# Optimization experiments

Measured on AMD Instinct MI355X. Metric: run time of the kernel, lower is better.

The kernel has to match this reference:

```python
import jax, jax.numpy as jnp
import numpy as np

B, N, M, D = 64, 197, 65, 768


def setup_inputs() -> dict:
    key = jax.random.key(0)
    k1, k2, k3 = jax.random.split(key, 3)
    image = jax.random.normal(k1, (B, N, D), dtype=jnp.float32)
    text = jax.random.normal(k2, (B, M, D), dtype=jnp.float32)
    pm = jax.random.randint(k3, (B, M), 0, 2).astype(jnp.int32)
    pm = pm.at[:, :2].set(0)  # CLS + first real token always valid
    logit_scale = jnp.ones((), dtype=jnp.float32)
    return {"image": image, "text": text, "padding_masks": pm, "logit_scale": logit_scale}


def _ce_with_diag_labels(logits):
    # F.cross_entropy(logits, arange(B)): mean of -log_softmax diag
    return -jnp.mean(jnp.diagonal(jax.nn.log_softmax(logits, axis=-1)))


def reference(image, text, padding_masks, logit_scale):
    # include_cls_token=False: original computes full [B,B,N,M] then slices
    # [:, :, 1:, 1:]; we compute the sliced tokens directly (same math).
    img = image[:, 1:, :]                   # [B, N-1, D]
    txt = text[:, 1:, :]                    # [B, M-1, D]
    pm = padding_masks[:, 1:].astype(bool)  # [B, M-1] True = padded

    # sim[i,j,n,m] = logit_scale * <img_i,n , txt_j,m>
    sim = logit_scale * jnp.einsum('ind,jmd->ijnm', img, txt)  # [B,B,N-1,M-1]

    # Original masks with NaN along mask of batch-row i (broadcast over j,n).
    # logits_per_image: nan_to_num(-inf) -> max over m -> mean over n
    sim_img = jnp.where(pm[:, None, None, :], -jnp.inf, sim)
    logits_per_image = jnp.mean(jnp.max(sim_img, axis=3), axis=2)  # [B,B]

    # logits_per_text: max over n (NaN cols stay NaN) -> nanmean over m.
    # Equivalent masked mean over valid m (mask constant along n).
    max_n = jnp.max(sim, axis=2)                         # [B,B,M-1]
    valid = ~pm                                          # [B,M-1]
    cnt = jnp.sum(valid, axis=1).astype(sim.dtype)       # [B]
    logits_per_text = jnp.sum(
        jnp.where(valid[:, None, :], max_n, 0.0), axis=2
    ) / cnt[:, None]                                     # [B,B]

    loss = 0.5 * (_ce_with_diag_labels(logits_per_image)
                  + _ce_with_diag_labels(logits_per_text))
    targets = jnp.arange(logits_per_image.shape[0], dtype=jnp.int32)
    return loss, logits_per_image, logits_per_text, targets
```

## Files before the change

### kernel.cpp

```cpp
#include <hip/hip_runtime.h>

typedef _Float16 half8 __attribute__((ext_vector_type(8)));
typedef float floatx4 __attribute__((ext_vector_type(4)));
typedef float float4v __attribute__((ext_vector_type(4)));

#define DIM   768
#define NROW  196
#define AUNITS (64 * 13 * 24 * 64)
#define TUNITS (64 * 4 * 24 * 64)
#define A_HALFS ((size_t)AUNITS * 8)
#define BJ_HALFS (24 * 4 * 64 * 8)

__device__ __forceinline__ void gl_lds16(const _Float16* g, _Float16* l) {
  __builtin_amdgcn_global_load_lds(
      (const __attribute__((address_space(1))) unsigned int*)g,
      (__attribute__((address_space(3))) unsigned int*)l, 16, 0, 0);
}

__global__ __launch_bounds__(256) void repack(const float* __restrict__ img,
                                              const float* __restrict__ txt,
                                              _Float16* __restrict__ Apk,
                                              _Float16* __restrict__ Bpk) {
  int gid = blockIdx.x * 256 + threadIdx.x;
  const float* src;
  _Float16* dst;
  if (gid < AUNITS) {
    int l = gid & 63, g = gid >> 6;
    int s = g % 24; g /= 24;
    int tau = g % 13; int i = g / 13;
    int n = tau * 16 + (l & 15); if (n > 195) n = 195;
    src = img + (size_t)i * 197 * 768 + (size_t)(n + 1) * 768 + s * 32 + (l >> 4) * 8;
    dst = Apk + (size_t)gid * 8;
  } else {
    int u = gid - AUNITS;
    int l = u & 63, g = u >> 6;
    int ct = g & 3; g >>= 2;
    int s = g % 24; int j = g / 24;
    int m = ct * 16 + (l & 15);
    src = txt + (size_t)j * 65 * 768 + (size_t)(m + 1) * 768 + s * 32 + (l >> 4) * 8;
    dst = Bpk + (size_t)u * 8;
  }
  float4v v0 = *(const float4v*)src;
  float4v v1 = *(const float4v*)(src + 4);
  half8 h;
  h[0] = (_Float16)v0[0]; h[1] = (_Float16)v0[1]; h[2] = (_Float16)v0[2]; h[3] = (_Float16)v0[3];
  h[4] = (_Float16)v1[0]; h[5] = (_Float16)v1[1]; h[6] = (_Float16)v1[2]; h[7] = (_Float16)v1[3];
  *(half8*)dst = h;
}

__global__ __launch_bounds__(256, 2) void sim_kernel(const _Float16* __restrict__ Apk,
                                                     const _Float16* __restrict__ Bpk,
                                                     const int* __restrict__ pm,
                                                     const float* __restrict__ ls,
                                                     float* __restrict__ lpi,
                                                     float* __restrict__ lpt) {
  __shared__ _Float16 Bsh[32768];

  const int jb = blockIdx.x, i = blockIdx.y;
  const int tid = threadIdx.x;
  const int wave = tid >> 6, lane = tid & 63;
  const int r16 = lane & 15;
  const int lane8 = lane * 8;

  const _Float16* Ai = Apk + (size_t)i * 13 * 24 * 512;
  const _Float16* pA[4];
  pA[0] = Ai + (size_t)(wave)     * 24 * 512 + lane8;
  pA[1] = Ai + (size_t)(wave + 4) * 24 * 512 + lane8;
  pA[2] = Ai + (size_t)(wave + 8) * 24 * 512 + lane8;
  pA[3] = Ai + (size_t)12         * 24 * 512 + lane8;
  const _Float16* Bg = Bpk + (size_t)(2 * jb) * BJ_HALFS;

#pragma unroll
  for (int r8 = 0; r8 < 8; ++r8) {
    int u = wave * 8 + r8;
    int jj = u >> 4, rr = u & 15;
    gl_lds16(Bg + (size_t)jj * BJ_HALFS + rr * 512 + lane8,
             Bsh + jj * 8192 + rr * 512);
  }

  half8 af[2][4];
#pragma unroll
  for (int d = 0; d < 2; ++d)
#pragma unroll
    for (int t = 0; t < 4; ++t)
      af[d][t] = *(const half8*)(pA[t] + d * 512);

  floatx4 acc[2][3][4];
  floatx4 acc12[2];
  acc12[0] = (floatx4){0.f, 0.f, 0.f, 0.f};
  acc12[1] = (floatx4){0.f, 0.f, 0.f, 0.f};
#pragma unroll
  for (int jj = 0; jj < 2; ++jj)
#pragma unroll
    for (int t = 0; t < 3; ++t)
#pragma unroll
      for (int cc = 0; cc < 4; ++cc)
        acc[jj][t][cc] = (floatx4){0.f, 0.f, 0.f, 0.f};

#pragma unroll
  for (int c = 0; c < 6; ++c) {
    __syncthreads();
    if (c < 5) {
#pragma unroll
      for (int r8 = 0; r8 < 8; ++r8) {
        int u = wave * 8 + r8;
        int jj = u >> 4, rr = u & 15;
        gl_lds16(Bg + (size_t)jj * BJ_HALFS + (c + 1) * 8192 + rr * 512 + lane8,
                 Bsh + ((c + 1) & 1) * 16384 + jj * 8192 + rr * 512);
      }
    }
#pragma unroll
    for (int sc = 0; sc < 4; ++sc) {
      const int s = c * 4 + sc;
      const int base = (c & 1) * 16384 + sc * 2048 + lane8;
      half8 b0[4], b1[4];
#pragma unroll
      for (int cc = 0; cc < 4; ++cc) {
        int ct = (wave + cc) & 3;
        b0[cc] = *(const half8*)(Bsh + base + ct * 512);
        b1[cc] = *(const half8*)(Bsh + base + 8192 + ct * 512);
      }
      half8 a0 = af[s & 1][0], a1 = af[s & 1][1], a2 = af[s & 1][2], a3 = af[s & 1][3];
      if (s < 22) {
#pragma unroll
        for (int t = 0; t < 4; ++t) af[s & 1][t] = *(const half8*)(pA[t] + (s + 2) * 512);
      }
#pragma unroll
      for (int cc = 0; cc < 4; ++cc) {
        acc[0][0][cc] = __builtin_amdgcn_mfma_f32_16x16x32_f16(a0, b0[cc], acc[0][0][cc], 0, 0, 0);
        acc[0][1][cc] = __builtin_amdgcn_mfma_f32_16x16x32_f16(a1, b0[cc], acc[0][1][cc], 0, 0, 0);
        acc[0][2][cc] = __builtin_amdgcn_mfma_f32_16x16x32_f16(a2, b0[cc], acc[0][2][cc], 0, 0, 0);
        acc[1][0][cc] = __builtin_amdgcn_mfma_f32_16x16x32_f16(a0, b1[cc], acc[1][0][cc], 0, 0, 0);
        acc[1][1][cc] = __builtin_amdgcn_mfma_f32_16x16x32_f16(a1, b1[cc], acc[1][1][cc], 0, 0, 0);
        acc[1][2][cc] = __builtin_amdgcn_mfma_f32_16x16x32_f16(a2, b1[cc], acc[1][2][cc], 0, 0, 0);
      }
      acc12[0] = __builtin_amdgcn_mfma_f32_16x16x32_f16(a3, b0[0], acc12[0], 0, 0, 0);
      acc12[1] = __builtin_amdgcn_mfma_f32_16x16x32_f16(a3, b1[0], acc12[1], 0, 0, 0);
    }
  }

  const float sgl = ls[0];
  bool msk[4];
  int colc[4];
#pragma unroll
  for (int cc = 0; cc < 4; ++cc) {
    colc[cc] = ((wave + cc) & 3) * 16 + r16;
    msk[cc] = pm[i * 65 + 1 + colc[cc]] != 0;
  }

  float rowsum[2] = {0.f, 0.f};
  float cmv[2][4];
#pragma unroll
  for (int jj = 0; jj < 2; ++jj) {
#pragma unroll
    for (int t = 0; t < 3; ++t) {
#pragma unroll
      for (int r = 0; r < 4; ++r) {
        float rm = -__builtin_inff();
#pragma unroll
        for (int cc = 0; cc < 4; ++cc) {
          float v = acc[jj][t][cc][r] * sgl;
          rm = fmaxf(rm, msk[cc] ? -__builtin_inff() : v);
        }
#pragma unroll
        for (int off = 1; off < 16; off <<= 1)
          rm = fmaxf(rm, __shfl_xor(rm, off, 64));
        rowsum[jj] += rm;
      }
    }
#pragma unroll
    for (int off = 1; off < 64; off <<= 1) rowsum[jj] += __shfl_xor(rowsum[jj], off, 64);

#pragma unroll
    for (int cc = 0; cc < 4; ++cc) {
      float cm = -__builtin_inff();
#pragma unroll
      for (int t = 0; t < 3; ++t)
#pragma unroll
        for (int r = 0; r < 4; ++r)
          cm = fmaxf(cm, acc[jj][t][cc][r] * sgl);
      cm = fmaxf(cm, __shfl_xor(cm, 16, 64));
      cm = fmaxf(cm, __shfl_xor(cm, 32, 64));
      cmv[jj][cc] = cm;
    }
  }

  __syncthreads();
  float* colmaxS = (float*)Bsh;
  float* t12S    = (float*)Bsh + 512;
  float* wsumS   = (float*)Bsh + 1024;

  if (lane == 0) { wsumS[wave] = rowsum[0]; wsumS[4 + wave] = rowsum[1]; }
  if (lane < 16) {
#pragma unroll
    for (int jj = 0; jj < 2; ++jj) {
#pragma unroll
      for (int cc = 0; cc < 4; ++cc) colmaxS[jj * 256 + wave * 64 + colc[cc]] = cmv[jj][cc];
#pragma unroll
      for (int r = 0; r < 4; ++r) t12S[jj * 256 + r * 64 + wave * 16 + r16] = acc12[jj][r] * sgl;
    }
  }
  __syncthreads();

  if (tid < 128) {
    const int jj = wave;
    const int col = lane;
    bool valid = pm[i * 65 + 1 + col] == 0;
    const float* cm = colmaxS + jj * 256;
    const float* t12 = t12S + jj * 256;
    float t0 = t12[col], t1 = t12[64 + col], t2 = t12[128 + col], t3 = t12[192 + col];
    float v = fmaxf(fmaxf(cm[col], cm[64 + col]), fmaxf(cm[128 + col], cm[192 + col]));
    v = fmaxf(v, fmaxf(fmaxf(t0, t1), fmaxf(t2, t3)));
    float contrib = valid ? v : 0.f;
    float cntv = valid ? 1.f : 0.f;
    float rs0 = valid ? t0 : -__builtin_inff();
    float rs1 = valid ? t1 : -__builtin_inff();
    float rs2 = valid ? t2 : -__builtin_inff();
    float rs3 = valid ? t3 : -__builtin_inff();
#pragma unroll
    for (int off = 1; off < 64; off <<= 1) {
      contrib += __shfl_xor(contrib, off, 64);
      cntv += __shfl_xor(cntv, off, 64);
      rs0 = fmaxf(rs0, __shfl_xor(rs0, off, 64));
      rs1 = fmaxf(rs1, __shfl_xor(rs1, off, 64));
      rs2 = fmaxf(rs2, __shfl_xor(rs2, off, 64));
      rs3 = fmaxf(rs3, __shfl_xor(rs3, off, 64));
    }
    if (lane == 0) {
      int jout = 2 * jb + jj;
      lpt[i * 64 + jout] = contrib / cntv;
      float wtot = wsumS[jj * 4 + 0] + wsumS[jj * 4 + 1] + wsumS[jj * 4 + 2] + wsumS[jj * 4 + 3];
      lpi[i * 64 + jout] = (wtot * 0.0625f + rs0 + rs1 + rs2 + rs3) / 196.f;
    }
  }
}

__global__ __launch_bounds__(64) void ce_kernel(float* __restrict__ out) {
  const int t = threadIdx.x;
  const float* lpi = out + 1;
  const float* lpt = out + 1 + 4096;

  float mx = -__builtin_inff();
  for (int jj = 0; jj < 64; ++jj) mx = fmaxf(mx, lpi[t * 64 + jj]);
  float se = 0.f;
  for (int jj = 0; jj < 64; ++jj) se += __expf(lpi[t * 64 + jj] - mx);
  float ci = (mx + __logf(se)) - lpi[t * 64 + t];

  float mx2 = -__builtin_inff();
  for (int jj = 0; jj < 64; ++jj) mx2 = fmaxf(mx2, lpt[t * 64 + jj]);
  float se2 = 0.f;
  for (int jj = 0; jj < 64; ++jj) se2 += __expf(lpt[t * 64 + jj] - mx2);
  float ct_ = (mx2 + __logf(se2)) - lpt[t * 64 + t];

  float v = ci + ct_;
#pragma unroll
  for (int off = 1; off < 64; off <<= 1) v += __shfl_xor(v, off, 64);
  if (t == 0) out[0] = 0.5f * v / 64.f;
  out[1 + 8192 + t] = (float)t;
}

extern "C" void kernel_launch(void* const* d_in, const int* in_sizes, int n_in,
                              void* d_out, int out_size, void* d_ws, size_t ws_size,
                              hipStream_t stream) {
  const float* image = (const float*)d_in[0];
  const float* text  = (const float*)d_in[1];
  const int*   pm    = (const int*)d_in[2];
  const float* ls    = (const float*)d_in[3];
  float* out = (float*)d_out;

  _Float16* Apk = (_Float16*)d_ws;
  _Float16* Bpk = Apk + A_HALFS;

  repack<<<(AUNITS + TUNITS) / 256, 256, 0, stream>>>(image, text, Apk, Bpk);

  dim3 grid(32, 64);
  sim_kernel<<<grid, 256, 0, stream>>>(Apk, Bpk, pm, ls, out + 1, out + 1 + 4096);
  ce_kernel<<<1, 64, 0, stream>>>(out);
}
```

Measured before the change: 185.7 us.

## Process one text batch per block to cut registers and LDS, raise occupancy

Each sim_kernel block now handles a single text item j instead of two. This halves the accumulator registers and shrinks LDS from 64KB to 16KB, with staging done in smaller double-buffered chunks over 12 stages. The grid doubles to 64x64 and launch bounds ask for 3 blocks per CU. The trade-off is that each image A tile is now reloaded from global/L2 twice as often, so every MFMA does less reuse. The ce_kernel loops are also unrolled.

Result: slower. 194.8 us (+4.9%).

```diff
diff --git a/kernel.cpp b/kernel.cpp
--- a/kernel.cpp
+++ b/kernel.cpp
@@ -48,15 +48,15 @@
   *(half8*)dst = h;
 }
 
-__global__ __launch_bounds__(256, 2) void sim_kernel(const _Float16* __restrict__ Apk,
+__global__ __launch_bounds__(256, 3) void sim_kernel(const _Float16* __restrict__ Apk,
                                                      const _Float16* __restrict__ Bpk,
                                                      const int* __restrict__ pm,
                                                      const float* __restrict__ ls,
                                                      float* __restrict__ lpi,
                                                      float* __restrict__ lpt) {
-  __shared__ _Float16 Bsh[32768];
-
-  const int jb = blockIdx.x, i = blockIdx.y;
+  __shared__ _Float16 Bsh[8192];
+
+  const int j = blockIdx.x, i = blockIdx.y;
   const int tid = threadIdx.x;
   const int wave = tid >> 6, lane = tid & 63;
   const int r16 = lane & 15;
@@ -68,14 +68,12 @@
   pA[1] = Ai + (size_t)(wave + 4) * 24 * 512 + lane8;
   pA[2] = Ai + (size_t)(wave + 8) * 24 * 512 + lane8;
   pA[3] = Ai + (size_t)12         * 24 * 512 + lane8;
-  const _Float16* Bg = Bpk + (size_t)(2 * jb) * BJ_HALFS;
-
-#pragma unroll
-  for (int r8 = 0; r8 < 8; ++r8) {
-    int u = wave * 8 + r8;
-    int jj = u >> 4, rr = u & 15;
-    gl_lds16(Bg + (size_t)jj * BJ_HALFS + rr * 512 + lane8,
-             Bsh + jj * 8192 + rr * 512);
+  const _Float16* Bg = Bpk + (size_t)j * BJ_HALFS;
+
+#pragma unroll
+  for (int r2 = 0; r2 < 2; ++r2) {
+    int rr = wave * 2 + r2;
+    gl_lds16(Bg + rr * 512 + lane8, Bsh + rr * 512);
   }
 
   half8 af[2][4];
@@ -85,40 +83,34 @@
     for (int t = 0; t < 4; ++t)
       af[d][t] = *(const half8*)(pA[t] + d * 512);
 
-  floatx4 acc[2][3][4];
-  floatx4 acc12[2];
-  acc12[0] = (floatx4){0.f, 0.f, 0.f, 0.f};
-  acc12[1] = (floatx4){0.f, 0.f, 0.f, 0.f};
-#pragma unroll
-  for (int jj = 0; jj < 2; ++jj)
-#pragma unroll
-    for (int t = 0; t < 3; ++t)
-#pragma unroll
-      for (int cc = 0; cc < 4; ++cc)
-        acc[jj][t][cc] = (floatx4){0.f, 0.f, 0.f, 0.f};
-
-#pragma unroll
-  for (int c = 0; c < 6; ++c) {
+  floatx4 acc[3][4];
+  floatx4 acc12 = (floatx4){0.f, 0.f, 0.f, 0.f};
+#pragma unroll
+  for (int t = 0; t < 3; ++t)
+#pragma unroll
+    for (int cc = 0; cc < 4; ++cc)
+      acc[t][cc] = (floatx4){0.f, 0.f, 0.f, 0.f};
+
+#pragma unroll
+  for (int c = 0; c < 12; ++c) {
     __syncthreads();
-    if (c < 5) {
-#pragma unroll
-      for (int r8 = 0; r8 < 8; ++r8) {
-        int u = wave * 8 + r8;
-        int jj = u >> 4, rr = u & 15;
-        gl_lds16(Bg + (size_t)jj * BJ_HALFS + (c + 1) * 8192 + rr * 512 + lane8,
-                 Bsh + ((c + 1) & 1) * 16384 + jj * 8192 + rr * 512);
-      }
-    }
-#pragma unroll
-    for (int sc = 0; sc < 4; ++sc) {
-      const int s = c * 4 + sc;
-      const int base = (c & 1) * 16384 + sc * 2048 + lane8;
-      half8 b0[4], b1[4];
+    if (c < 11) {
+#pragma unroll
+      for (int r2 = 0; r2 < 2; ++r2) {
+        int rr = wave * 2 + r2;
+        gl_lds16(Bg + (c + 1) * 4096 + rr * 512 + lane8,
+                 Bsh + ((c + 1) & 1) * 4096 + rr * 512);
+      }
+    }
+#pragma unroll
+    for (int sc = 0; sc < 2; ++sc) {
+      const int s = c * 2 + sc;
+      const int base = (c & 1) * 4096 + sc * 2048 + lane8;
+      half8 b0[4];
 #pragma unroll
       for (int cc = 0; cc < 4; ++cc) {
         int ct = (wave + cc) & 3;
         b0[cc] = *(const half8*)(Bsh + base + ct * 512);
-        b1[cc] = *(const half8*)(Bsh + base + 8192 + ct * 512);
       }
       half8 a0 = af[s & 1][0], a1 = af[s & 1][1], a2 = af[s & 1][2], a3 = af[s & 1][3];
       if (s < 22) {
@@ -127,15 +119,11 @@
       }
 #pragma unroll
       for (int cc = 0; cc < 4; ++cc) {
-        acc[0][0][cc] = __builtin_amdgcn_mfma_f32_16x16x32_f16(a0, b0[cc], acc[0][0][cc], 0, 0, 0);
-        acc[0][1][cc] = __builtin_amdgcn_mfma_f32_16x16x32_f16(a1, b0[cc], acc[0][1][cc], 0, 0, 0);
-        acc[0][2][cc] = __builtin_amdgcn_mfma_f32_16x16x32_f16(a2, b0[cc], acc[0][2][cc], 0, 0, 0);
-        acc[1][0][cc] = __builtin_amdgcn_mfma_f32_16x16x32_f16(a0, b1[cc], acc[1][0][cc], 0, 0, 0);
-        acc[1][1][cc] = __builtin_amdgcn_mfma_f32_16x16x32_f16(a1, b1[cc], acc[1][1][cc], 0, 0, 0);
-        acc[1][2][cc] = __builtin_amdgcn_mfma_f32_16x16x32_f16(a2, b1[cc], acc[1][2][cc], 0, 0, 0);
-      }
-      acc12[0] = __builtin_amdgcn_mfma_f32_16x16x32_f16(a3, b0[0], acc12[0], 0, 0, 0);
-      acc12[1] = __builtin_amdgcn_mfma_f32_16x16x32_f16(a3, b1[0], acc12[1], 0, 0, 0);
+        acc[0][cc] = __builtin_amdgcn_mfma_f32_16x16x32_f16(a0, b0[cc], acc[0][cc], 0, 0, 0);
+        acc[1][cc] = __builtin_amdgcn_mfma_f32_16x16x32_f16(a1, b0[cc], acc[1][cc], 0, 0, 0);
+        acc[2][cc] = __builtin_amdgcn_mfma_f32_16x16x32_f16(a2, b0[cc], acc[2][cc], 0, 0, 0);
+      }
+      acc12 = __builtin_amdgcn_mfma_f32_16x16x32_f16(a3, b0[0], acc12, 0, 0, 0);
     }
   }
 
@@ -148,68 +136,60 @@
     msk[cc] = pm[i * 65 + 1 + colc[cc]] != 0;
   }
 
-  float rowsum[2] = {0.f, 0.f};
-  float cmv[2][4];
-#pragma unroll
-  for (int jj = 0; jj < 2; ++jj) {
-#pragma unroll
-    for (int t = 0; t < 3; ++t) {
-#pragma unroll
-      for (int r = 0; r < 4; ++r) {
-        float rm = -__builtin_inff();
-#pragma unroll
-        for (int cc = 0; cc < 4; ++cc) {
-          float v = acc[jj][t][cc][r] * sgl;
-          rm = fmaxf(rm, msk[cc] ? -__builtin_inff() : v);
-        }
-#pragma unroll
-        for (int off = 1; off < 16; off <<= 1)
-          rm = fmaxf(rm, __shfl_xor(rm, off, 64));
-        rowsum[jj] += rm;
-      }
-    }
-#pragma unroll
-    for (int off = 1; off < 64; off <<= 1) rowsum[jj] += __shfl_xor(rowsum[jj], off, 64);
-
-#pragma unroll
-    for (int cc = 0; cc < 4; ++cc) {
-      float cm = -__builtin_inff();
-#pragma unroll
-      for (int t = 0; t < 3; ++t)
-#pragma unroll
-        for (int r = 0; r < 4; ++r)
-          cm = fmaxf(cm, acc[jj][t][cc][r] * sgl);
-      cm = fmaxf(cm, __shfl_xor(cm, 16, 64));
-      cm = fmaxf(cm, __shfl_xor(cm, 32, 64));
-      cmv[jj][cc] = cm;
-    }
+  float rowsum = 0.f;
+  float cmv[4];
+#pragma unroll
+  for (int t = 0; t < 3; ++t) {
+#pragma unroll
+    for (int r = 0; r < 4; ++r) {
+      float rm = -__builtin_inff();
+#pragma unroll
+      for (int cc = 0; cc < 4; ++cc) {
+        float v = acc[t][cc][r] * sgl;
+        rm = fmaxf(rm, msk[cc] ? -__builtin_inff() : v);
+      }
+#pragma unroll
+      for (int off = 1; off < 16; off <<= 1)
+        rm = fmaxf(rm, __shfl_xor(rm, off, 64));
+      rowsum += rm;
+    }
+  }
+#pragma unroll
+  for (int off = 1; off < 64; off <<= 1) rowsum += __shfl_xor(rowsum, off, 64);
+
+#pragma unroll
+  for (int cc = 0; cc < 4; ++cc) {
+    float cm = -__builtin_inff();
+#pragma unroll
+    for (int t = 0; t < 3; ++t)
+#pragma unroll
+      for (int r = 0; r < 4; ++r)
+        cm = fmaxf(cm, acc[t][cc][r] * sgl);
+    cm = fmaxf(cm, __shfl_xor(cm, 16, 64));
+    cm = fmaxf(cm, __shfl_xor(cm, 32, 64));
+    cmv[cc] = cm;
   }
 
   __syncthreads();
   float* colmaxS = (float*)Bsh;
-  float* t12S    = (float*)Bsh + 512;
-  float* wsumS   = (float*)Bsh + 1024;
-
-  if (lane == 0) { wsumS[wave] = rowsum[0]; wsumS[4 + wave] = rowsum[1]; }
+  float* t12S    = (float*)Bsh + 256;
+  float* wsumS   = (float*)Bsh + 512;
+
+  if (lane == 0) wsumS[wave] = rowsum;
   if (lane < 16) {
 #pragma unroll
-    for (int jj = 0; jj < 2; ++jj) {
-#pragma unroll
-      for (int cc = 0; cc < 4; ++cc) colmaxS[jj * 256 + wave * 64 + colc[cc]] = cmv[jj][cc];
-#pragma unroll
-      for (int r = 0; r < 4; ++r) t12S[jj * 256 + r * 64 + wave * 16 + r16] = acc12[jj][r] * sgl;
-    }
+    for (int cc = 0; cc < 4; ++cc) colmaxS[wave * 64 + colc[cc]] = cmv[cc];
+#pragma unroll
+    for (int r = 0; r < 4; ++r) t12S[r * 64 + wave * 16 + r16] = acc12[r] * sgl;
   }
   __syncthreads();
 
-  if (tid < 128) {
-    const int jj = wave;
+  if (tid < 64) {
     const int col = lane;
     bool valid = pm[i * 65 + 1 + col] == 0;
-    const float* cm = colmaxS + jj * 256;
-    const float* t12 = t12S + jj * 256;
-    float t0 = t12[col], t1 = t12[64 + col], t2 = t12[128 + col], t3 = t12[192 + col];
-    float v = fmaxf(fmaxf(cm[col], cm[64 + col]), fmaxf(cm[128 + col], cm[192 + col]));
+    float t0 = t12S[col], t1 = t12S[64 + col], t2 = t12S[128 + col], t3 = t12S[192 + col];
+    float v = fmaxf(fmaxf(colmaxS[col], colmaxS[64 + col]),
+                    fmaxf(colmaxS[128 + col], colmaxS[192 + col]));
     v = fmaxf(v, fmaxf(fmaxf(t0, t1), fmaxf(t2, t3)));
     float contrib = valid ? v : 0.f;
     float cntv = valid ? 1.f : 0.f;
@@ -227,10 +207,9 @@
       rs3 = fmaxf(rs3, __shfl_xor(rs3, off, 64));
     }
     if (lane == 0) {
-      int jout = 2 * jb + jj;
-      lpt[i * 64 + jout] = contrib / cntv;
-      float wtot = wsumS[jj * 4 + 0] + wsumS[jj * 4 + 1] + wsumS[jj * 4 + 2] + wsumS[jj * 4 + 3];
-      lpi[i * 64 + jout] = (wtot * 0.0625f + rs0 + rs1 + rs2 + rs3) / 196.f;
+      lpt[i * 64 + j] = contrib / cntv;
+      float wtot = wsumS[0] + wsumS[1] + wsumS[2] + wsumS[3];
+      lpi[i * 64 + j] = (wtot * 0.0625f + rs0 + rs1 + rs2 + rs3) / 196.f;
     }
   }
 }
@@ -241,14 +220,18 @@
   const float* lpt = out + 1 + 4096;
 
   float mx = -__builtin_inff();
+#pragma unroll
   for (int jj = 0; jj < 64; ++jj) mx = fmaxf(mx, lpi[t * 64 + jj]);
   float se = 0.f;
+#pragma unroll
   for (int jj = 0; jj < 64; ++jj) se += __expf(lpi[t * 64 + jj] - mx);
   float ci = (mx + __logf(se)) - lpi[t * 64 + t];
 
   float mx2 = -__builtin_inff();
+#pragma unroll
   for (int jj = 0; jj < 64; ++jj) mx2 = fmaxf(mx2, lpt[t * 64 + jj]);
   float se2 = 0.f;
+#pragma unroll
   for (int jj = 0; jj < 64; ++jj) se2 += __expf(lpt[t * 64 + jj] - mx2);
   float ct_ = (mx2 + __logf(se2)) - lpt[t * 64 + t];
 
@@ -273,7 +256,7 @@
 
   repack<<<(AUNITS + TUNITS) / 256, 256, 0, stream>>>(image, text, Apk, Bpk);
 
-  dim3 grid(32, 64);
+  dim3 grid(64, 64);
   sim_kernel<<<grid, 256, 0, stream>>>(Apk, Bpk, pm, ls, out + 1, out + 1 + 4096);
   ce_kernel<<<1, 64, 0, stream>>>(out);
 }
```
